# Optimization experiments

Measured on AMD Instinct MI355X. Metric: run time of the kernel, lower is better.

## Reference

```python
import jax, jax.numpy as jnp
import numpy as np
import math

B, T, C, H = 2, 1024, 1024, 16
D = C // H


def setup_inputs() -> dict:
    key = jax.random.key(0)
    ks = jax.random.split(key, 7)
    scale = 1.0 / math.sqrt(C)
    q = jax.random.normal(ks[0], (B, T, C), dtype=jnp.float32)
    k = jax.random.normal(ks[1], (B, T, C), dtype=jnp.float32)
    v = jax.random.normal(ks[2], (B, T, C), dtype=jnp.float32)
    # causal mask, True = masked out (matches create_causal_mask)
    mask = jnp.triu(jnp.ones((T, T), dtype=bool), k=1)[None, None]
    Wk = jax.random.normal(ks[3], (C, C), dtype=jnp.float32) * scale
    bk = jax.random.normal(ks[4], (C,), dtype=jnp.float32) * scale
    Wc = jax.random.normal(ks[5], (C, C), dtype=jnp.float32) * scale
    bc = jax.random.normal(ks[6], (C,), dtype=jnp.float32) * scale
    return {"q": q, "k": k, "v": v, "mask": mask, "Wk": Wk, "bk": bk, "Wc": Wc, "bc": bc}


def reference(q, k, v, mask, Wk, bk, Wc, bc):
    # NOTE: original module uses self.k_attn for ALL of q, k, v (q_attn/v_attn unused).
    qB, qT, qC = q.shape
    kT = k.shape[1]
    qp = (q @ Wk.T + bk).reshape(qB, qT, H, D).transpose(0, 2, 1, 3)  # [B,H,Tq,D]
    kp = (k @ Wk.T + bk).reshape(qB, kT, H, D).transpose(0, 2, 1, 3)  # [B,H,Tk,D]
    vp = (v @ Wk.T + bk).reshape(qB, kT, H, D).transpose(0, 2, 1, 3)  # [B,H,Tk,D]
    att = jnp.einsum('bhqd,bhkd->bhqk', qp, kp) * (1.0 / math.sqrt(D))
    att = jnp.where(mask, -jnp.inf, att)
    att = jax.nn.softmax(att, axis=-1)
    y = jnp.einsum('bhqk,bhkd->bhqd', att, vp)
    y = y.transpose(0, 2, 1, 3).reshape(qB, qT, qC)
    return y @ Wc.T + bc
```

## Files before the change

kernel.cpp:

```cpp
#include <hip/hip_runtime.h>

#define T_DIM 1024
#define C_DIM 1024
#define H_DIM 16
#define D_DIM 64
#define KD    1024

typedef short  short8  __attribute__((ext_vector_type(8)));
typedef short  short4v __attribute__((ext_vector_type(4)));
typedef float  f32x4   __attribute__((ext_vector_type(4)));

__device__ __forceinline__ float bf2f(short s) {
  return __uint_as_float(((unsigned)(unsigned short)s) << 16);
}
__device__ __forceinline__ short f2bf(float f) {
  unsigned u = __float_as_uint(f);
  u += 0x7fffu + ((u >> 16) & 1u);
  return (short)(u >> 16);
}
__device__ __forceinline__ unsigned pk2(float lo, float hi) {
  return ((unsigned)(unsigned short)f2bf(lo)) | (((unsigned)(unsigned short)f2bf(hi)) << 16);
}

__device__ __forceinline__ void gl2lds16(const short* g, short* l) {
  __builtin_amdgcn_global_load_lds(
      (const __attribute__((address_space(1))) unsigned int*)(const void*)g,
      (__attribute__((address_space(3))) unsigned int*)(void*)l,
      16, 0, 0);
}

__device__ __forceinline__ short8 ldfrag(const void* p, size_t off, int isf32) {
  if (isf32) {
    const float* q = (const float*)p + off;
    f32x4 lo = *(const f32x4*)q;
    f32x4 hi = *(const f32x4*)(q + 4);
    short8 r;
#pragma unroll
    for (int j = 0; j < 4; ++j) { r[j] = f2bf(lo[j]); r[j + 4] = f2bf(hi[j]); }
    return r;
  }
  return *(const short8*)((const short*)p + off);
}
__device__ __forceinline__ float ldbias(const void* b, int i, int isf32) {
  return isf32 ? ((const float*)b)[i] : bf2f(((const short*)b)[i]);
}

__device__ __forceinline__ int detect_f32_inblock(const unsigned* w, int lane) {
  int c = 0;
#pragma unroll
  for (int i = 0; i < 4; ++i) {
    unsigned e = (w[lane * 4 + i] >> 7) & 0xffu;
    c += (e >= 110u && e <= 135u) ? 1 : 0;
  }
#pragma unroll
  for (int off = 32; off; off >>= 1) c += __shfl_xor(c, off);
  return (c < 128) ? 1 : 0;
}

#define SZE  ((size_t)2 * T_DIM * C_DIM)
#define QN   ((size_t)2097152)
#define WN   ((size_t)1048576)
#define BN   ((size_t)1024)
#define CVT_TOT (3 * QN + 2 * WN + 2 * BN)

__global__ __launch_bounds__(256) void cvt_k(const void* __restrict__ q,
                                             const void* __restrict__ k,
                                             const void* __restrict__ v,
                                             const void* __restrict__ wk,
                                             const void* __restrict__ wc,
                                             const void* __restrict__ bk,
                                             const void* __restrict__ bc,
                                             short* __restrict__ dst)
{
  const int lane = threadIdx.x & 63;
  const int f = detect_f32_inblock((const unsigned*)q, lane);

  const size_t idx = (size_t)blockIdx.x * 1024 + threadIdx.x * 4;
  if (idx >= CVT_TOT) return;
  const void* src;
  size_t loc;
  if      (idx <     QN)          { src = q;  loc = idx; }
  else if (idx < 2 * QN)          { src = k;  loc = idx - QN; }
  else if (idx < 3 * QN)          { src = v;  loc = idx - 2 * QN; }
  else if (idx < 3 * QN + WN)     { src = wk; loc = idx - 3 * QN; }
  else if (idx < 3 * QN + 2 * WN) { src = wc; loc = idx - 3 * QN - WN; }
  else if (idx < 3 * QN + 2 * WN + BN) { src = bk; loc = idx - 3 * QN - 2 * WN; }
  else                            { src = bc; loc = idx - 3 * QN - 2 * WN - BN; }

  short4v o;
  if (f) {
    f32x4 x = *(const f32x4*)((const float*)src + loc);
#pragma unroll
    for (int j = 0; j < 4; ++j) o[j] = f2bf(x[j]);
  } else {
    o = *(const short4v*)((const short*)src + loc);
  }
  *(short4v*)(dst + idx) = o;
}

__device__ __forceinline__ void stage8x8(const short* gsrc, short* S, int R0,
                                         int lane, int koff) {
  const int rw = R0 + (lane >> 3);
  const int q  = (lane & 7) ^ (rw & 7);
  gl2lds16(gsrc + (size_t)rw * KD + koff + q * 8, &S[R0 * 64]);
}
__device__ __forceinline__ short8 fragread64(const short* S, int row, int chunk) {
  const int sl = (row << 3) + (chunk ^ (row & 7));
  return *(const short8*)&S[sl << 3];
}

__global__ __launch_bounds__(256) void gemm_qkv_a(const short* __restrict__ X0,
                                                  const short* __restrict__ X1,
                                                  const short* __restrict__ X2,
                                                  const short* __restrict__ Wv,
                                                  const short* __restrict__ Bv,
                                                  short* __restrict__ outv)
{
  const int tid  = threadIdx.x;
  const int lane = tid & 63;
  const int wave = tid >> 6;
  const int col16 = lane & 15;
  const int quad  = lane >> 4;

  const int m0 = blockIdx.x * 128;
  const int c0 = blockIdx.y * 64;

  const int src = m0 >> 11;
  const short* Xv = (src == 0) ? X0 : (src == 1) ? X1 : X2;
  const int arow = m0 & 2047;
  const bool isv = (src == 2);
  short* outb = outv + (size_t)src * SZE;

  __shared__ short As[128 * 64];
  __shared__ short Bs[64 * 64];

  const short* Xg = Xv + (size_t)arow * KD;
  const short* Wg = Wv + (size_t)c0 * KD;

  f32x4 acc[2][4] = {};

  for (int k0 = 0; k0 < KD; k0 += 64) {
    if (k0) __syncthreads();
    stage8x8(Xg, As, wave * 32,      lane, k0);
    stage8x8(Xg, As, wave * 32 + 8,  lane, k0);
    stage8x8(Xg, As, wave * 32 + 16, lane, k0);
    stage8x8(Xg, As, wave * 32 + 24, lane, k0);
    stage8x8(Wg, Bs, wave * 16,      lane, k0);
    stage8x8(Wg, Bs, wave * 16 + 8,  lane, k0);
    __syncthreads();

#pragma unroll
    for (int kk = 0; kk < 2; ++kk) {
      short8 fx[2], fw[4];
#pragma unroll
      for (int i = 0; i < 2; ++i)
        fx[i] = fragread64(As, wave * 32 + i * 16 + col16, kk * 4 + quad);
#pragma unroll
      for (int j = 0; j < 4; ++j)
        fw[j] = fragread64(Bs, j * 16 + col16, kk * 4 + quad);

      if (isv) {
#pragma unroll
        for (int i = 0; i < 2; ++i)
#pragma unroll
          for (int j = 0; j < 4; ++j)
            acc[i][j] = __builtin_amdgcn_mfma_f32_16x16x32_bf16(fx[i], fw[j], acc[i][j], 0, 0, 0);
      } else {
#pragma unroll
        for (int i = 0; i < 2; ++i)
#pragma unroll
          for (int j = 0; j < 4; ++j)
            acc[i][j] = __builtin_amdgcn_mfma_f32_16x16x32_bf16(fw[j], fx[i], acc[i][j], 0, 0, 0);
      }
    }
  }

  if (isv) {
#pragma unroll
    for (int i = 0; i < 2; ++i) {
#pragma unroll
      for (int j = 0; j < 4; ++j) {
        const int c  = c0 + j * 16 + col16;
        const int t0 = arow + wave * 32 + i * 16 + quad * 4;
        const float bv = bf2f(Bv[c]);
        short4v pk;
#pragma unroll
        for (int r = 0; r < 4; ++r) pk[r] = f2bf(acc[i][j][r] + bv);
        const int bb = t0 >> 10, t = t0 & 1023, h = c >> 6, d = c & 63;
        size_t off = (size_t)((bb * H_DIM + h) * D_DIM + d) * T_DIM + t;
        *(short4v*)(outb + off) = pk;
      }
    }
  } else {
#pragma unroll
    for (int i = 0; i < 2; ++i) {
#pragma unroll
      for (int j = 0; j < 4; ++j) {
        const int m  = arow + wave * 32 + i * 16 + col16;
        const int cb = c0 + j * 16 + quad * 4;
        short4v bv4 = *(const short4v*)(Bv + cb);
        short4v pk;
#pragma unroll
        for (int r = 0; r < 4; ++r) pk[r] = f2bf(acc[i][j][r] + bf2f(bv4[r]));
        const int bb = m >> 10, t = m & 1023, h = cb >> 6, d = cb & 63;
        size_t off = ((size_t)(bb * H_DIM + h) << 16) + (size_t)t * D_DIM + d;
        *(short4v*)(outb + off) = pk;
      }
    }
  }
}

__global__ __launch_bounds__(256) void gemm_out_a(const short* __restrict__ Xb,
                                                  const short* __restrict__ Wv,
                                                  const short* __restrict__ Bv,
                                                  float* __restrict__ outv)
{
  const int tid  = threadIdx.x;
  const int lane = tid & 63;
  const int wave = tid >> 6;
  const int col16 = lane & 15;
  const int quad  = lane >> 4;
  const int wm = wave & 1;
  const int wn = wave >> 1;

  const int m0 = blockIdx.x * 64;
  const int c0 = blockIdx.y * 64;

  __shared__ short As[64 * 64];
  __shared__ short Bs[64 * 64];

  const short* Xg = Xb + (size_t)m0 * KD;
  const short* Wg = Wv + (size_t)c0 * KD;

  f32x4 acc[2][2] = {};

  for (int k0 = 0; k0 < KD; k0 += 64) {
    if (k0) __syncthreads();
    stage8x8(Xg, As, wave * 16,     lane, k0);
    stage8x8(Xg, As, wave * 16 + 8, lane, k0);
    stage8x8(Wg, Bs, wave * 16,     lane, k0);
    stage8x8(Wg, Bs, wave * 16 + 8, lane, k0);
    __syncthreads();

#pragma unroll
    for (int kk = 0; kk < 2; ++kk) {
      short8 fx[2], fw[2];
#pragma unroll
      for (int i = 0; i < 2; ++i)
        fx[i] = fragread64(As, wm * 32 + i * 16 + col16, kk * 4 + quad);
#pragma unroll
      for (int j = 0; j < 2; ++j)
        fw[j] = fragread64(Bs, wn * 32 + j * 16 + col16, kk * 4 + quad);

#pragma unroll
      for (int i = 0; i < 2; ++i)
#pragma unroll
        for (int j = 0; j < 2; ++j)
          acc[i][j] = __builtin_amdgcn_mfma_f32_16x16x32_bf16(fw[j], fx[i], acc[i][j], 0, 0, 0);
    }
  }

#pragma unroll
  for (int i = 0; i < 2; ++i) {
#pragma unroll
    for (int j = 0; j < 2; ++j) {
      const int m  = m0 + wm * 32 + i * 16 + col16;
      const int cb = c0 + wn * 32 + j * 16 + quad * 4;
      f32x4 pv;
#pragma unroll
      for (int r = 0; r < 4; ++r) pv[r] = acc[i][j][r] + bf2f(Bv[cb + r]);
      *(f32x4*)(outv + (size_t)m * C_DIM + cb) = pv;
    }
  }
}

#define LDSP 40

template<int KIND>
__global__ __launch_bounds__(256) void gemm2_k(const void* __restrict__ X0,
                                               const void* __restrict__ X1,
                                               const void* __restrict__ X2,
                                               const void* __restrict__ Wv,
                                               const void* __restrict__ Bv,
                                               void* __restrict__ outv)
{
  const int tid  = threadIdx.x;
  const int lane = tid & 63;
  const int wave = tid >> 6;
  const int col16 = lane & 15;
  const int quad  = lane >> 4;
  const int wm = wave & 1;
  const int wn = wave >> 1;

  const int f  = detect_f32_inblock((const unsigned*)Wv, lane);
  const int wf = f;
  const int xf = (KIND == 1) ? f : 0;

  const int m0 = blockIdx.x * 64;
  const int c0 = blockIdx.y * 64;

  const void* Xv = X0;
  int arow = m0;
  bool isv = false;
  short* outb = (short*)outv;
  if (KIND == 1) {
    const int src = m0 >> 11;
    Xv = (src == 0) ? X0 : (src == 1) ? X1 : X2;
    arow = m0 & 2047;
    isv = (src == 2);
    outb = (short*)outv + (size_t)src * SZE;
  }

  __shared__ short As[64 * LDSP];
  __shared__ short Bs[64 * LDSP];

  const int srow = tid >> 2;
  const int sc8  = tid & 3;

  f32x4 acc[2][2] = {};

  for (int k0 = 0; k0 < KD; k0 += 32) {
    short8 va = ldfrag(Xv, (size_t)(arow + srow) * KD + k0 + sc8 * 8, xf);
    short8 vb = ldfrag(Wv, (size_t)(c0 + srow) * KD + k0 + sc8 * 8, wf);
    if (k0) __syncthreads();
    *(short8*)&As[srow * LDSP + sc8 * 8] = va;
    *(short8*)&Bs[srow * LDSP + sc8 * 8] = vb;
    __syncthreads();

    short8 fx[2], fw[2];
#pragma unroll
    for (int i = 0; i < 2; ++i)
      fx[i] = *(const short8*)&As[(wm * 32 + i * 16 + col16) * LDSP + quad * 8];
#pragma unroll
    for (int j = 0; j < 2; ++j)
      fw[j] = *(const short8*)&Bs[(wn * 32 + j * 16 + col16) * LDSP + quad * 8];

    if (KIND == 1 && isv) {
#pragma unroll
      for (int i = 0; i < 2; ++i)
#pragma unroll
        for (int j = 0; j < 2; ++j)
          acc[i][j] = __builtin_amdgcn_mfma_f32_16x16x32_bf16(fx[i], fw[j], acc[i][j], 0, 0, 0);
    } else {
#pragma unroll
      for (int i = 0; i < 2; ++i)
#pragma unroll
        for (int j = 0; j < 2; ++j)
          acc[i][j] = __builtin_amdgcn_mfma_f32_16x16x32_bf16(fw[j], fx[i], acc[i][j], 0, 0, 0);
    }
  }

  if (KIND == 1 && isv) {
#pragma unroll
    for (int i = 0; i < 2; ++i) {
#pragma unroll
      for (int j = 0; j < 2; ++j) {
        const int c  = c0 + wn * 32 + j * 16 + col16;
        const int t0 = arow + wm * 32 + i * 16 + quad * 4;
        const float bv = ldbias(Bv, c, wf);
        short4v pk;
#pragma unroll
        for (int r = 0; r < 4; ++r) pk[r] = f2bf(acc[i][j][r] + bv);
        const int bb = t0 >> 10, t = t0 & 1023, h = c >> 6, d = c & 63;
        size_t off = (size_t)((bb * H_DIM + h) * D_DIM + d) * T_DIM + t;
        *(short4v*)(outb + off) = pk;
      }
    }
  } else {
#pragma unroll
    for (int i = 0; i < 2; ++i) {
#pragma unroll
      for (int j = 0; j < 2; ++j) {
        const int m  = arow + wm * 32 + i * 16 + col16;
        const int cb = c0 + wn * 32 + j * 16 + quad * 4;
        if (KIND == 0) {
          f32x4 pv;
#pragma unroll
          for (int r = 0; r < 4; ++r) pv[r] = acc[i][j][r] + ldbias(Bv, cb + r, wf);
          *(f32x4*)((float*)outv + (size_t)m * C_DIM + cb) = pv;
        } else {
          short4v pk;
#pragma unroll
          for (int r = 0; r < 4; ++r) pk[r] = f2bf(acc[i][j][r] + ldbias(Bv, cb + r, wf));
          const int bb = m >> 10, t = m & 1023, h = cb >> 6, d = cb & 63;
          size_t off = ((size_t)(bb * H_DIM + h) << 16) + (size_t)t * D_DIM + d;
          *(short4v*)(outb + off) = pk;
        }
      }
    }
  }
}

__global__ __launch_bounds__(256) void attn_k3(const short* __restrict__ qp,
                                               const short* __restrict__ kp,
                                               const short* __restrict__ vpt,
                                               short* __restrict__ y)
{
  const int lane = threadIdx.x & 63;
  const int wave = threadIdx.x >> 6;
  const int col  = lane & 15;
  const int quad = lane >> 4;
  const int bh = blockIdx.x;
  const int b = bh >> 4, h = bh & 15;
  const int qt = 63 - (int)blockIdx.y;
  const int q0 = qt * 16;
  const int myq = q0 + col;

  const short* qph = qp  + (size_t)bh * (T_DIM * D_DIM);
  const short* kph = kp  + (size_t)bh * (T_DIM * D_DIM);
  const short* vph = vpt + (size_t)bh * (D_DIM * T_DIM);

  const int nkt  = (q0 + 47) >> 5;
  const int base = nkt >> 2, rem = nkt & 3;
  const int cnt   = base + (wave < rem ? 1 : 0);
  const int start = wave * base + (wave < rem ? wave : rem);

  short8 bQ[2];
#pragma unroll
  for (int kk = 0; kk < 2; ++kk)
    bQ[kk] = *(const short8*)(qph + (size_t)(q0 + col) * D_DIM + kk * 32 + quad * 8);

  f32x4 O[4] = {};
  float rs = 0.0f;

  const int slA = col + ((quad & 1) * 32);
  const int slB = slA + 16;

#pragma unroll 2
  for (int kt = start; kt < start + cnt; ++kt) {
    const int kb = kt * 32;
    f32x4 st[2];
#pragma unroll
    for (int jt = 0; jt < 2; ++jt) {
      f32x4 s = {0.f, 0.f, 0.f, 0.f};
      const short* kbase = kph + (size_t)(kb + jt * 16 + col) * D_DIM + quad * 8;
      short8 aK0 = *(const short8*)(kbase);
      short8 aK1 = *(const short8*)(kbase + 32);
      s = __builtin_amdgcn_mfma_f32_16x16x32_bf16(aK0, bQ[0], s, 0, 0, 0);
      s = __builtin_amdgcn_mfma_f32_16x16x32_bf16(aK1, bQ[1], s, 0, 0, 0);
      st[jt] = s;
    }
#pragma unroll
    for (int jt = 0; jt < 2; ++jt) {
#pragma unroll
      for (int r = 0; r < 4; ++r) {
        const int key = kb + jt * 16 + quad * 4 + r;
        float p = __expf(st[jt][r] * 0.125f);
        p = (key > myq) ? 0.0f : p;
        st[jt][r] = p;
        rs += p;
      }
    }

    const int a0 = (int)pk2(st[0][0], st[0][1]);
    const int a1 = (int)pk2(st[0][2], st[0][3]);
    const int b0 = (int)pk2(st[1][0], st[1][1]);
    const int b1 = (int)pk2(st[1][2], st[1][3]);
    const int tA0 = __shfl(a0, slA, 64), tB0 = __shfl(b0, slA, 64);
    const int tA1 = __shfl(a1, slA, 64), tB1 = __shfl(b1, slA, 64);
    const int tA2 = __shfl(a0, slB, 64), tB2 = __shfl(b0, slB, 64);
    const int tA3 = __shfl(a1, slB, 64), tB3 = __shfl(b1, slB, 64);
    union { unsigned u[4]; short8 s8; } uu;
    uu.u[0] = (unsigned)((quad < 2) ? tA0 : tB0);
    uu.u[1] = (unsigned)((quad < 2) ? tA1 : tB1);
    uu.u[2] = (unsigned)((quad < 2) ? tA2 : tB2);
    uu.u[3] = (unsigned)((quad < 2) ? tA3 : tB3);
    const short8 bP32 = uu.s8;

#pragma unroll
    for (int dt = 0; dt < 4; ++dt) {
      short8 aV = *(const short8*)(vph + (size_t)(dt * 16 + col) * T_DIM + kb + quad * 8);
      O[dt] = __builtin_amdgcn_mfma_f32_16x16x32_bf16(aV, bP32, O[dt], 0, 0, 0);
    }
  }

  rs += __shfl_xor(rs, 16);
  rs += __shfl_xor(rs, 32);

  __shared__ float Om[4 * 4 * 16 * 16];
  __shared__ float Ll[4][16];

#pragma unroll
  for (int dt = 0; dt < 4; ++dt)
    *(f32x4*)&Om[(((wave * 4 + dt) * 16) + col) * 16 + quad * 4] = O[dt];
  if (quad == 0) Ll[wave][col] = rs;
  __syncthreads();

  float L = Ll[0][col] + Ll[1][col] + Ll[2][col] + Ll[3][col];
  f32x4 oacc = {0.f, 0.f, 0.f, 0.f};
#pragma unroll
  for (int w = 0; w < 4; ++w) {
    f32x4 ov = *(const f32x4*)&Om[(((w * 4 + wave) * 16) + col) * 16 + quad * 4];
#pragma unroll
    for (int r = 0; r < 4; ++r) oacc[r] += ov[r];
  }
  const float rl = 1.0f / L;
  const int t = q0 + col;
  const size_t ybase = ((size_t)(b * T_DIM + t)) * C_DIM + h * D_DIM + quad * 4;
  short4v pk;
#pragma unroll
  for (int r = 0; r < 4; ++r) pk[r] = f2bf(oacc[r] * rl);
  *(short4v*)(y + ybase + wave * 16) = pk;
}

extern "C" void kernel_launch(void* const* d_in, const int* in_sizes, int n_in,
                              void* d_out, int out_size, void* d_ws, size_t ws_size,
                              hipStream_t stream) {
  const void* q = d_in[0];
  const void* k = d_in[1];
  const void* v = d_in[2];
  int wi = (n_in >= 8 && in_sizes[4] == C_DIM * C_DIM) ? 4 : 3;
  const void* Wk = d_in[wi];
  const void* bk = d_in[wi + 1];
  const void* Wc = d_in[wi + 2];
  const void* bc = d_in[wi + 3];

  short* ws  = (short*)d_ws;
  short* qp  = ws;
  short* kp  = ws + SZE;
  short* vpt = ws + 2 * SZE;
  short* y   = ws + 3 * SZE;

  short* ext = ws + 4 * SZE;
  const size_t needed = (4 * SZE + CVT_TOT) * sizeof(short);
  const bool pre = (ws_size >= needed);

  dim3 blk(256);
  if (pre) {
    cvt_k<<<dim3((unsigned)((CVT_TOT + 1023) / 1024)), blk, 0, stream>>>(
        q, k, v, Wk, Wc, bk, bc, ext);
    const short* gq  = ext;
    const short* gk  = ext + QN;
    const short* gv  = ext + 2 * QN;
    const short* gwk = ext + 3 * QN;
    const short* gwc = ext + 3 * QN + WN;
    const short* gbk = ext + 3 * QN + 2 * WN;
    const short* gbc = ext + 3 * QN + 2 * WN + BN;

    gemm_qkv_a<<<dim3(48, 16), blk, 0, stream>>>(gq, gk, gv, gwk, gbk, qp);
    attn_k3<<<dim3(32, 64), blk, 0, stream>>>(qp, kp, vpt, y);
    gemm_out_a<<<dim3(32, 16), blk, 0, stream>>>(y, gwc, gbc, (float*)d_out);
  } else {
    gemm2_k<1><<<dim3(96, 16), blk, 0, stream>>>(q, k, v, Wk, bk, qp);
    attn_k3<<<dim3(32, 64), blk, 0, stream>>>(qp, kp, vpt, y);
    gemm2_k<0><<<dim3(32, 16), blk, 0, stream>>>(y, nullptr, nullptr, Wc, bc, d_out);
  }
}
```

Baseline: 157.9 us.

## Enlarge QKV GEMM tile to 128x128 with 2x2 wave layout; prioritize attention MFMAs

The QKV projection GEMM now computes 128x128 output tiles per block, using a 2x2 wave arrangement with 4x4 MFMA accumulators per wave. This halves the grid along the column dimension and raises arithmetic intensity per LDS load. In the attention kernel, the V fragment loads are hoisted ahead of the PV MFMAs, and both MFMA groups are wrapped in s_setprio to favor matrix issue across waves. The trade-off is higher register and LDS use, which can lower occupancy, and a grid of 384 blocks instead of 768.

```diff
diff --git a/kernel.cpp b/kernel.cpp
--- a/kernel.cpp
+++ b/kernel.cpp
@@ -121,9 +121,11 @@
   const int wave = tid >> 6;
   const int col16 = lane & 15;
   const int quad  = lane >> 4;
+  const int wm = wave & 1;
+  const int wn = wave >> 1;
 
   const int m0 = blockIdx.x * 128;
-  const int c0 = blockIdx.y * 64;
+  const int c0 = blockIdx.y * 128;
 
   const int src = m0 >> 11;
   const short* Xv = (src == 0) ? X0 : (src == 1) ? X1 : X2;
@@ -132,12 +134,12 @@
   short* outb = outv + (size_t)src * SZE;
 
   __shared__ short As[128 * 64];
-  __shared__ short Bs[64 * 64];
+  __shared__ short Bs[128 * 64];
 
   const short* Xg = Xv + (size_t)arow * KD;
   const short* Wg = Wv + (size_t)c0 * KD;
 
-  f32x4 acc[2][4] = {};
+  f32x4 acc[4][4] = {};
 
   for (int k0 = 0; k0 < KD; k0 += 64) {
     if (k0) __syncthreads();
@@ -145,29 +147,31 @@
     stage8x8(Xg, As, wave * 32 + 8,  lane, k0);
     stage8x8(Xg, As, wave * 32 + 16, lane, k0);
     stage8x8(Xg, As, wave * 32 + 24, lane, k0);
-    stage8x8(Wg, Bs, wave * 16,      lane, k0);
-    stage8x8(Wg, Bs, wave * 16 + 8,  lane, k0);
+    stage8x8(Wg, Bs, wave * 32,      lane, k0);
+    stage8x8(Wg, Bs, wave * 32 + 8,  lane, k0);
+    stage8x8(Wg, Bs, wave * 32 + 16, lane, k0);
+    stage8x8(Wg, Bs, wave * 32 + 24, lane, k0);
     __syncthreads();
 
 #pragma unroll
     for (int kk = 0; kk < 2; ++kk) {
-      short8 fx[2], fw[4];
-#pragma unroll
-      for (int i = 0; i < 2; ++i)
-        fx[i] = fragread64(As, wave * 32 + i * 16 + col16, kk * 4 + quad);
+      short8 fx[4], fw[4];
+#pragma unroll
+      for (int i = 0; i < 4; ++i)
+        fx[i] = fragread64(As, wm * 64 + i * 16 + col16, kk * 4 + quad);
 #pragma unroll
       for (int j = 0; j < 4; ++j)
-        fw[j] = fragread64(Bs, j * 16 + col16, kk * 4 + quad);
+        fw[j] = fragread64(Bs, wn * 64 + j * 16 + col16, kk * 4 + quad);
 
       if (isv) {
 #pragma unroll
-        for (int i = 0; i < 2; ++i)
+        for (int i = 0; i < 4; ++i)
 #pragma unroll
           for (int j = 0; j < 4; ++j)
             acc[i][j] = __builtin_amdgcn_mfma_f32_16x16x32_bf16(fx[i], fw[j], acc[i][j], 0, 0, 0);
       } else {
 #pragma unroll
-        for (int i = 0; i < 2; ++i)
+        for (int i = 0; i < 4; ++i)
 #pragma unroll
           for (int j = 0; j < 4; ++j)
             acc[i][j] = __builtin_amdgcn_mfma_f32_16x16x32_bf16(fw[j], fx[i], acc[i][j], 0, 0, 0);
@@ -177,11 +181,11 @@
 
   if (isv) {
 #pragma unroll
-    for (int i = 0; i < 2; ++i) {
+    for (int i = 0; i < 4; ++i) {
 #pragma unroll
       for (int j = 0; j < 4; ++j) {
-        const int c  = c0 + j * 16 + col16;
-        const int t0 = arow + wave * 32 + i * 16 + quad * 4;
+        const int c  = c0 + wn * 64 + j * 16 + col16;
+        const int t0 = arow + wm * 64 + i * 16 + quad * 4;
         const float bv = bf2f(Bv[c]);
         short4v pk;
 #pragma unroll
@@ -193,11 +197,11 @@
     }
   } else {
 #pragma unroll
-    for (int i = 0; i < 2; ++i) {
+    for (int i = 0; i < 4; ++i) {
 #pragma unroll
       for (int j = 0; j < 4; ++j) {
-        const int m  = arow + wave * 32 + i * 16 + col16;
-        const int cb = c0 + j * 16 + quad * 4;
+        const int m  = arow + wm * 64 + i * 16 + col16;
+        const int cb = c0 + wn * 64 + j * 16 + quad * 4;
         short4v bv4 = *(const short4v*)(Bv + cb);
         short4v pk;
 #pragma unroll
@@ -436,8 +440,10 @@
       const short* kbase = kph + (size_t)(kb + jt * 16 + col) * D_DIM + quad * 8;
       short8 aK0 = *(const short8*)(kbase);
       short8 aK1 = *(const short8*)(kbase + 32);
+      __builtin_amdgcn_s_setprio(1);
       s = __builtin_amdgcn_mfma_f32_16x16x32_bf16(aK0, bQ[0], s, 0, 0, 0);
       s = __builtin_amdgcn_mfma_f32_16x16x32_bf16(aK1, bQ[1], s, 0, 0, 0);
+      __builtin_amdgcn_s_setprio(0);
       st[jt] = s;
     }
 #pragma unroll
@@ -467,11 +473,15 @@
     uu.u[3] = (unsigned)((quad < 2) ? tA3 : tB3);
     const short8 bP32 = uu.s8;
 
-#pragma unroll
-    for (int dt = 0; dt < 4; ++dt) {
-      short8 aV = *(const short8*)(vph + (size_t)(dt * 16 + col) * T_DIM + kb + quad * 8);
-      O[dt] = __builtin_amdgcn_mfma_f32_16x16x32_bf16(aV, bP32, O[dt], 0, 0, 0);
-    }
+    short8 aV[4];
+#pragma unroll
+    for (int dt = 0; dt < 4; ++dt)
+      aV[dt] = *(const short8*)(vph + (size_t)(dt * 16 + col) * T_DIM + kb + quad * 8);
+    __builtin_amdgcn_s_setprio(1);
+#pragma unroll
+    for (int dt = 0; dt < 4; ++dt)
+      O[dt] = __builtin_amdgcn_mfma_f32_16x16x32_bf16(aV[dt], bP32, O[dt], 0, 0, 0);
+    __builtin_amdgcn_s_setprio(0);
   }
 
   rs += __shfl_xor(rs, 16);
@@ -537,7 +547,7 @@
     const short* gbk = ext + 3 * QN + 2 * WN;
     const short* gbc = ext + 3 * QN + 2 * WN + BN;
 
-    gemm_qkv_a<<<dim3(48, 16), blk, 0, stream>>>(gq, gk, gv, gwk, gbk, qp);
+    gemm_qkv_a<<<dim3(48, 8), blk, 0, stream>>>(gq, gk, gv, gwk, gbk, qp);
     attn_k3<<<dim3(32, 64), blk, 0, stream>>>(qp, kp, vpt, y);
     gemm_out_a<<<dim3(32, 16), blk, 0, stream>>>(y, gwc, gbc, (float*)d_out);
   } else {
```

After: 164.3 us. 1.04x slower.
